# Optimization experiments

Measured on AMD Instinct MI355X. Metric: run time of the kernel, lower is better.

Reference implementation:

```python
import jax, jax.numpy as jnp
import numpy as np

N, IN_CH, OUT_CH, E = 16384, 512, 512, 8


def setup_inputs() -> dict:
    key = jax.random.key(0)
    k1, k2, k3, k4 = jax.random.split(key, 4)
    x = jax.random.normal(k1, (N, IN_CH), dtype=jnp.float32)
    coefficients = jax.random.uniform(k2, (N, E), dtype=jnp.float32)
    # kaiming-uniform-ish init: bound = 1/sqrt(fan_in)
    bound = 1.0 / np.sqrt(IN_CH)
    weight = jax.random.uniform(k3, (E, OUT_CH, IN_CH), minval=-bound, maxval=bound, dtype=jnp.float32)
    bias = jax.random.uniform(k4, (E, OUT_CH), minval=-bound, maxval=bound, dtype=jnp.float32)
    return {"x": x, "coefficients": coefficients, "weight": weight, "bias": bias}


def reference(x, coefficients, weight, bias):
    # Original: mixed_weight = einsum('bc,cmn->bmn', coef, W); out = baddbmm(mixed_bias, mixed_weight, x)
    # Equivalent (by bilinearity) without materializing the (N,out,in) tensor:
    # per-expert matvec combined with coefficients in one einsum.
    out = jnp.einsum('ne,eoi,ni->no', coefficients, weight, x)
    out = out + coefficients @ bias  # (N,E) @ (E,out) -> (N,out)
    return out
```

## Files before the change

### kernel.cpp

```cpp
#include <hip/hip_runtime.h>

#define N_TOK 16384
#define CIN   512
#define COUT  512
#define NE    8
#define BM    256
#define BN    128
#define BK    64
#define KTILES   64

typedef __attribute__((ext_vector_type(8))) short bf16x8;
typedef __attribute__((ext_vector_type(4))) short s16x4;
typedef __attribute__((ext_vector_type(4))) float f32x4;

__device__ __forceinline__ short f2bf(float f) {
  unsigned u = __builtin_bit_cast(unsigned, f);
  u += 0x7FFFu + ((u >> 16) & 1u);
  return (short)(u >> 16);
}

__global__ void cvt_all(const float4* __restrict__ x, const float4* __restrict__ w,
                        s16x4* __restrict__ xb, s16x4* __restrict__ wb) {
  int i = blockIdx.x * blockDim.x + threadIdx.x;
  const int NX = N_TOK * CIN / 4;
  float4 v; s16x4* o;
  if (i < NX) { v = x[i]; o = xb + i; }
  else       { int j = i - NX; v = w[j]; o = wb + j; }
  s16x4 r;
  r[0] = f2bf(v.x); r[1] = f2bf(v.y); r[2] = f2bf(v.z); r[3] = f2bf(v.w);
  *o = r;
}

__device__ __forceinline__ void async16(short* lds, const short* g) {
  __builtin_amdgcn_global_load_lds(
      (const __attribute__((address_space(1))) void*)g,
      (__attribute__((address_space(3))) void*)lds, 16, 0, 0);
}

__global__ __launch_bounds__(512, 2)
void moe_gemm(const short* __restrict__ xb,
              const short* __restrict__ wb,
              const float* __restrict__ coef,
              const float* __restrict__ bias,
              float* __restrict__ out) {
  __shared__ short As[3][BM * BK];
  __shared__ short Bs[3][BN * BK];
  __shared__ float cf[BM * NE];

  const int tid  = threadIdx.x;
  const int lane = tid & 63;
  const int wid  = tid >> 6;
  const int wm   = wid >> 2;
  const int wn   = wid & 3;
  const int lhi  = lane >> 4;
  const int llo  = lane & 15;

  const int bid  = blockIdx.x;
  const int ct   = bid & 3;
  const int rt   = bid >> 2;
  const int row0 = rt * BM;
  const int col0 = ct * BN;

  ((float4*)cf)[tid] = ((const float4*)(coef + row0 * NE))[tid];

  const int r_st = tid >> 3;
  const int c_sw = ((tid & 7) * 8) ^ ((r_st & 7) << 3);
  const short* gA = xb + (row0 + r_st) * CIN + c_sw;
  const short* gB = wb + (col0 + r_st) * CIN + c_sw;

  auto stageA = [&](int buf, int t, int p) {
    const int i0 = (t & 7) * BK;
    async16(&As[buf][p * 4096 + tid * 8], gA + p * 64 * CIN + i0);
  };
  auto stageB = [&](int buf, int t, int p) {
    const int e  = t >> 3;
    const int i0 = (t & 7) * BK;
    async16(&Bs[buf][p * 4096 + tid * 8], gB + e * (CIN * COUT) + p * 64 * CIN + i0);
  };

  const int swz0 = (lhi * 8) ^ ((llo & 7) << 3);
  const int swz1 = (32 + lhi * 8) ^ ((llo & 7) << 3);
  const int arow = wm * 128 + llo;
  const int brow = wn * 32 + llo;

  f32x4 accO[8][2], accE[8][2];
#pragma unroll
  for (int m = 0; m < 8; ++m)
#pragma unroll
    for (int n = 0; n < 2; ++n) {
      accO[m][n] = (f32x4){0.f, 0.f, 0.f, 0.f};
      accE[m][n] = (f32x4){0.f, 0.f, 0.f, 0.f};
    }

#pragma unroll
  for (int p = 0; p < 4; ++p) stageA(0, 0, p);
#pragma unroll
  for (int p = 0; p < 2; ++p) stageB(0, 0, p);
#pragma unroll
  for (int p = 0; p < 4; ++p) stageA(1, 1, p);
#pragma unroll
  for (int p = 0; p < 2; ++p) stageB(1, 1, p);
  asm volatile("s_waitcnt vmcnt(6) lgkmcnt(0)");
  __builtin_amdgcn_s_barrier();

  bf16x8 bfr[2][2];

  for (int t = 0; t < KTILES; ++t) {
    const int cur = t % 3;
    const int nx  = (t + 2) % 3;
    const bool pf = (t + 2) < KTILES;
    const short* Ab = As[cur];
    const short* Bb = Bs[cur];

#pragma unroll
    for (int p = 0; p < 4; ++p) {
      bf16x8 af[2][2];
      af[0][0] = *(const bf16x8*)&Ab[(arow + (2 * p) * 16) * 64 + swz0];
      af[0][1] = *(const bf16x8*)&Ab[(arow + (2 * p) * 16) * 64 + swz1];
      af[1][0] = *(const bf16x8*)&Ab[(arow + (2 * p + 1) * 16) * 64 + swz0];
      af[1][1] = *(const bf16x8*)&Ab[(arow + (2 * p + 1) * 16) * 64 + swz1];
      if (p == 0) {
        bfr[0][0] = *(const bf16x8*)&Bb[(brow + 0) * 64 + swz0];
        bfr[0][1] = *(const bf16x8*)&Bb[(brow + 0) * 64 + swz1];
        bfr[1][0] = *(const bf16x8*)&Bb[(brow + 16) * 64 + swz0];
        bfr[1][1] = *(const bf16x8*)&Bb[(brow + 16) * 64 + swz1];
      }
      if (pf) {
        if (p == 0)      { stageA(nx, t + 2, 0); stageA(nx, t + 2, 1); }
        else if (p == 1) { stageA(nx, t + 2, 2); stageA(nx, t + 2, 3); }
        else if (p == 2) { stageB(nx, t + 2, 0); stageB(nx, t + 2, 1); }
      }
      __builtin_amdgcn_s_barrier();
      asm volatile("s_waitcnt lgkmcnt(0)");
      __builtin_amdgcn_s_setprio(1);
#pragma unroll
      for (int mm = 0; mm < 2; ++mm)
#pragma unroll
        for (int n = 0; n < 2; ++n)
#pragma unroll
          for (int ks = 0; ks < 2; ++ks)
            accE[2 * p + mm][n] = __builtin_amdgcn_mfma_f32_16x16x32_bf16(
                af[mm][ks], bfr[n][ks], accE[2 * p + mm][n], 0, 0, 0);
      __builtin_amdgcn_s_setprio(0);
      __builtin_amdgcn_s_barrier();
    }

    if ((t & 7) == 7) {
      const int e = t >> 3;
#pragma unroll
      for (int m = 0; m < 8; ++m)
#pragma unroll
        for (int r = 0; r < 4; ++r) {
          float c = cf[(wm * 128 + m * 16 + lhi * 4 + r) * NE + e];
#pragma unroll
          for (int n = 0; n < 2; ++n) {
            accO[m][n][r] += c * accE[m][n][r];
            accE[m][n][r] = 0.f;
          }
        }
    }

    if (t < KTILES - 2) {
      asm volatile("s_waitcnt vmcnt(6)");
      __builtin_amdgcn_s_barrier();
    } else if (t == KTILES - 2) {
      asm volatile("s_waitcnt vmcnt(0)");
      __builtin_amdgcn_s_barrier();
    }
  }

  float bcol[2][NE];
#pragma unroll
  for (int n = 0; n < 2; ++n) {
    const int cg = col0 + wn * 32 + n * 16 + llo;
#pragma unroll
    for (int e = 0; e < NE; ++e) bcol[n][e] = bias[e * COUT + cg];
  }
#pragma unroll
  for (int m = 0; m < 8; ++m)
#pragma unroll
    for (int r = 0; r < 4; ++r) {
      const int rl = wm * 128 + m * 16 + lhi * 4 + r;
      float cv[NE];
#pragma unroll
      for (int e = 0; e < NE; ++e) cv[e] = cf[rl * NE + e];
      float* orow = out + (size_t)(row0 + rl) * COUT;
#pragma unroll
      for (int n = 0; n < 2; ++n) {
        float bm = 0.f;
#pragma unroll
        for (int e = 0; e < NE; ++e) bm += cv[e] * bcol[n][e];
        orow[col0 + wn * 32 + n * 16 + llo] = accO[m][n][r] + bm;
      }
    }
}

extern "C" void kernel_launch(void* const* d_in, const int* in_sizes, int n_in,
                              void* d_out, int out_size, void* d_ws, size_t ws_size,
                              hipStream_t stream) {
  const float* x    = (const float*)d_in[0];
  const float* coef = (const float*)d_in[1];
  const float* w    = (const float*)d_in[2];
  const float* bias = (const float*)d_in[3];
  float* out = (float*)d_out;

  short* xb = (short*)d_ws;
  short* wb = xb + (size_t)N_TOK * CIN;

  const int NX = N_TOK * CIN / 4, NW = NE * COUT * CIN / 4;
  cvt_all<<<(NX + NW) / 256, 256, 0, stream>>>(
      (const float4*)x, (const float4*)w, (s16x4*)xb, (s16x4*)wb);

  moe_gemm<<<(N_TOK / BM) * (COUT / BN), 512, 0, stream>>>(xb, wb, coef, bias, out);
}
```

Measured before the change: 192.5 us.

## Fold expert coefficients via Horner-style ratio rescaling, single accumulator set

Replaces the separate per-expert accumulator plus coefficient-weighted sum with one accumulator set. After each expert, the running sum is rescaled by the ratio c_e/c_{e+1}, and the last expert's coefficient is applied at the end. Precomputed ratios live in shared memory. The change also swaps the wave layout to 4x2 with 64x64 wave tiles, drops from triple to double buffering with a full vmcnt wait every tile, and adds a block-index swizzle. Fewer accumulator registers and less epilogue FMA work come at the cost of weaker load/compute overlap. Numerical risk: coefficients are clamped to 1e-20, and small coefficients give large ratios, so results depend on coefficients being positive and not near zero.

```diff
diff --git a/kernel.cpp b/kernel.cpp
--- a/kernel.cpp
+++ b/kernel.cpp
@@ -7,7 +7,7 @@
 #define BM    256
 #define BN    128
 #define BK    64
-#define KTILES   64
+#define KTILES 64
 
 typedef __attribute__((ext_vector_type(8))) short bf16x8;
 typedef __attribute__((ext_vector_type(4))) short s16x4;
@@ -43,154 +43,164 @@
               const float* __restrict__ coef,
               const float* __restrict__ bias,
               float* __restrict__ out) {
-  __shared__ short As[3][BM * BK];
-  __shared__ short Bs[3][BN * BK];
-  __shared__ float cf[BM * NE];
+  __shared__ short As[2][BM * BK];
+  __shared__ short Bs[2][BN * BK];
+  __shared__ float cfc[BM * NE];
+  __shared__ float cfr[BM * NE];
 
   const int tid  = threadIdx.x;
   const int lane = tid & 63;
   const int wid  = tid >> 6;
-  const int wm   = wid >> 2;
-  const int wn   = wid & 3;
+  const int wm   = wid >> 1;
+  const int wn   = wid & 1;
   const int lhi  = lane >> 4;
   const int llo  = lane & 15;
 
-  const int bid  = blockIdx.x;
+  const int bid0 = blockIdx.x;
+  const int bid  = (bid0 & 7) * 32 + (bid0 >> 3);
   const int ct   = bid & 3;
   const int rt   = bid >> 2;
   const int row0 = rt * BM;
   const int col0 = ct * BN;
 
-  ((float4*)cf)[tid] = ((const float4*)(coef + row0 * NE))[tid];
+  ((float4*)cfc)[tid] = ((const float4*)(coef + row0 * NE))[tid];
 
   const int r_st = tid >> 3;
   const int c_sw = ((tid & 7) * 8) ^ ((r_st & 7) << 3);
-  const short* gA = xb + (row0 + r_st) * CIN + c_sw;
-  const short* gB = wb + (col0 + r_st) * CIN + c_sw;
-
-  auto stageA = [&](int buf, int t, int p) {
-    const int i0 = (t & 7) * BK;
-    async16(&As[buf][p * 4096 + tid * 8], gA + p * 64 * CIN + i0);
-  };
-  auto stageB = [&](int buf, int t, int p) {
+  const short* gA = xb + (size_t)(row0 + r_st) * CIN + c_sw;
+  const short* gB = wb + (size_t)(col0 + r_st) * CIN + c_sw;
+
+  auto stage = [&](int buf, int t) {
     const int e  = t >> 3;
     const int i0 = (t & 7) * BK;
-    async16(&Bs[buf][p * 4096 + tid * 8], gB + e * (CIN * COUT) + p * 64 * CIN + i0);
+#pragma unroll
+    for (int p = 0; p < 4; ++p)
+      async16(&As[buf][p * 4096 + tid * 8], gA + p * 64 * CIN + i0);
+#pragma unroll
+    for (int p = 0; p < 2; ++p)
+      async16(&Bs[buf][p * 4096 + tid * 8], gB + (size_t)e * (CIN * COUT) + p * 64 * CIN + i0);
   };
+
+  stage(0, 0);
+  asm volatile("s_waitcnt lgkmcnt(0)");
+  __builtin_amdgcn_s_barrier();
+  if (tid < BM) {
+    const float* cp = &cfc[tid * NE];
+    float c[NE];
+#pragma unroll
+    for (int e = 0; e < NE; ++e) c[e] = fmaxf(cp[e], 1e-20f);
+    float* rp = &cfr[tid * NE];
+#pragma unroll
+    for (int e = 0; e < NE - 1; ++e) rp[e] = c[e] / c[e + 1];
+    rp[NE - 1] = c[NE - 1];
+  }
+  asm volatile("s_waitcnt vmcnt(0) lgkmcnt(0)");
+  __builtin_amdgcn_s_barrier();
 
   const int swz0 = (lhi * 8) ^ ((llo & 7) << 3);
   const int swz1 = (32 + lhi * 8) ^ ((llo & 7) << 3);
-  const int arow = wm * 128 + llo;
-  const int brow = wn * 32 + llo;
-
-  f32x4 accO[8][2], accE[8][2];
-#pragma unroll
-  for (int m = 0; m < 8; ++m)
-#pragma unroll
-    for (int n = 0; n < 2; ++n) {
-      accO[m][n] = (f32x4){0.f, 0.f, 0.f, 0.f};
-      accE[m][n] = (f32x4){0.f, 0.f, 0.f, 0.f};
-    }
-
-#pragma unroll
-  for (int p = 0; p < 4; ++p) stageA(0, 0, p);
-#pragma unroll
-  for (int p = 0; p < 2; ++p) stageB(0, 0, p);
-#pragma unroll
-  for (int p = 0; p < 4; ++p) stageA(1, 1, p);
-#pragma unroll
-  for (int p = 0; p < 2; ++p) stageB(1, 1, p);
-  asm volatile("s_waitcnt vmcnt(6) lgkmcnt(0)");
-  __builtin_amdgcn_s_barrier();
-
-  bf16x8 bfr[2][2];
+  const int arow = wm * 64 + llo;
+  const int brow = wn * 64 + llo;
+
+  f32x4 acc[4][4];
+#pragma unroll
+  for (int m = 0; m < 4; ++m)
+#pragma unroll
+    for (int n = 0; n < 4; ++n)
+      acc[m][n] = (f32x4){0.f, 0.f, 0.f, 0.f};
 
   for (int t = 0; t < KTILES; ++t) {
-    const int cur = t % 3;
-    const int nx  = (t + 2) % 3;
-    const bool pf = (t + 2) < KTILES;
+    const int cur = t & 1;
     const short* Ab = As[cur];
     const short* Bb = Bs[cur];
 
-#pragma unroll
-    for (int p = 0; p < 4; ++p) {
-      bf16x8 af[2][2];
-      af[0][0] = *(const bf16x8*)&Ab[(arow + (2 * p) * 16) * 64 + swz0];
-      af[0][1] = *(const bf16x8*)&Ab[(arow + (2 * p) * 16) * 64 + swz1];
-      af[1][0] = *(const bf16x8*)&Ab[(arow + (2 * p + 1) * 16) * 64 + swz0];
-      af[1][1] = *(const bf16x8*)&Ab[(arow + (2 * p + 1) * 16) * 64 + swz1];
-      if (p == 0) {
-        bfr[0][0] = *(const bf16x8*)&Bb[(brow + 0) * 64 + swz0];
-        bfr[0][1] = *(const bf16x8*)&Bb[(brow + 0) * 64 + swz1];
-        bfr[1][0] = *(const bf16x8*)&Bb[(brow + 16) * 64 + swz0];
-        bfr[1][1] = *(const bf16x8*)&Bb[(brow + 16) * 64 + swz1];
-      }
-      if (pf) {
-        if (p == 0)      { stageA(nx, t + 2, 0); stageA(nx, t + 2, 1); }
-        else if (p == 1) { stageA(nx, t + 2, 2); stageA(nx, t + 2, 3); }
-        else if (p == 2) { stageB(nx, t + 2, 0); stageB(nx, t + 2, 1); }
-      }
-      __builtin_amdgcn_s_barrier();
-      asm volatile("s_waitcnt lgkmcnt(0)");
-      __builtin_amdgcn_s_setprio(1);
-#pragma unroll
-      for (int mm = 0; mm < 2; ++mm)
-#pragma unroll
-        for (int n = 0; n < 2; ++n)
-#pragma unroll
-          for (int ks = 0; ks < 2; ++ks)
-            accE[2 * p + mm][n] = __builtin_amdgcn_mfma_f32_16x16x32_bf16(
-                af[mm][ks], bfr[n][ks], accE[2 * p + mm][n], 0, 0, 0);
-      __builtin_amdgcn_s_setprio(0);
-      __builtin_amdgcn_s_barrier();
-    }
+    if (t + 1 < KTILES) stage(cur ^ 1, t + 1);
+    bf16x8 bf[4][2];
+#pragma unroll
+    for (int n = 0; n < 4; ++n) {
+      bf[n][0] = *(const bf16x8*)&Bb[(brow + n * 16) * 64 + swz0];
+      bf[n][1] = *(const bf16x8*)&Bb[(brow + n * 16) * 64 + swz1];
+    }
+    bf16x8 af[2][2];
+#pragma unroll
+    for (int mm = 0; mm < 2; ++mm) {
+      af[mm][0] = *(const bf16x8*)&Ab[(arow + mm * 16) * 64 + swz0];
+      af[mm][1] = *(const bf16x8*)&Ab[(arow + mm * 16) * 64 + swz1];
+    }
+    __builtin_amdgcn_s_barrier();
+    asm volatile("s_waitcnt lgkmcnt(0)");
+    __builtin_amdgcn_s_setprio(1);
+#pragma unroll
+    for (int mm = 0; mm < 2; ++mm)
+#pragma unroll
+      for (int n = 0; n < 4; ++n)
+#pragma unroll
+        for (int ks = 0; ks < 2; ++ks)
+          acc[mm][n] = __builtin_amdgcn_mfma_f32_16x16x32_bf16(
+              af[mm][ks], bf[n][ks], acc[mm][n], 0, 0, 0);
+    __builtin_amdgcn_s_setprio(0);
+    __builtin_amdgcn_s_barrier();
+
+#pragma unroll
+    for (int mm = 0; mm < 2; ++mm) {
+      af[mm][0] = *(const bf16x8*)&Ab[(arow + (2 + mm) * 16) * 64 + swz0];
+      af[mm][1] = *(const bf16x8*)&Ab[(arow + (2 + mm) * 16) * 64 + swz1];
+    }
+    __builtin_amdgcn_s_barrier();
+    asm volatile("s_waitcnt lgkmcnt(0)");
+    __builtin_amdgcn_s_setprio(1);
+#pragma unroll
+    for (int mm = 0; mm < 2; ++mm)
+#pragma unroll
+      for (int n = 0; n < 4; ++n)
+#pragma unroll
+        for (int ks = 0; ks < 2; ++ks)
+          acc[2 + mm][n] = __builtin_amdgcn_mfma_f32_16x16x32_bf16(
+              af[mm][ks], bf[n][ks], acc[2 + mm][n], 0, 0, 0);
+    __builtin_amdgcn_s_setprio(0);
+    __builtin_amdgcn_s_barrier();
 
     if ((t & 7) == 7) {
       const int e = t >> 3;
 #pragma unroll
-      for (int m = 0; m < 8; ++m)
+      for (int m = 0; m < 4; ++m)
 #pragma unroll
         for (int r = 0; r < 4; ++r) {
-          float c = cf[(wm * 128 + m * 16 + lhi * 4 + r) * NE + e];
-#pragma unroll
-          for (int n = 0; n < 2; ++n) {
-            accO[m][n][r] += c * accE[m][n][r];
-            accE[m][n][r] = 0.f;
-          }
+          float rr = cfr[(wm * 64 + m * 16 + lhi * 4 + r) * NE + e];
+#pragma unroll
+          for (int n = 0; n < 4; ++n)
+            acc[m][n][r] *= rr;
         }
     }
 
-    if (t < KTILES - 2) {
-      asm volatile("s_waitcnt vmcnt(6)");
-      __builtin_amdgcn_s_barrier();
-    } else if (t == KTILES - 2) {
+    if (t + 1 < KTILES) {
       asm volatile("s_waitcnt vmcnt(0)");
       __builtin_amdgcn_s_barrier();
     }
   }
 
-  float bcol[2][NE];
-#pragma unroll
-  for (int n = 0; n < 2; ++n) {
-    const int cg = col0 + wn * 32 + n * 16 + llo;
+  float bcol[4][NE];
+#pragma unroll
+  for (int n = 0; n < 4; ++n) {
+    const int cg = col0 + wn * 64 + n * 16 + llo;
 #pragma unroll
     for (int e = 0; e < NE; ++e) bcol[n][e] = bias[e * COUT + cg];
   }
 #pragma unroll
-  for (int m = 0; m < 8; ++m)
+  for (int m = 0; m < 4; ++m)
 #pragma unroll
     for (int r = 0; r < 4; ++r) {
-      const int rl = wm * 128 + m * 16 + lhi * 4 + r;
+      const int rl = wm * 64 + m * 16 + lhi * 4 + r;
       float cv[NE];
 #pragma unroll
-      for (int e = 0; e < NE; ++e) cv[e] = cf[rl * NE + e];
+      for (int e = 0; e < NE; ++e) cv[e] = cfc[rl * NE + e];
       float* orow = out + (size_t)(row0 + rl) * COUT;
 #pragma unroll
-      for (int n = 0; n < 2; ++n) {
+      for (int n = 0; n < 4; ++n) {
         float bm = 0.f;
 #pragma unroll
         for (int e = 0; e < NE; ++e) bm += cv[e] * bcol[n][e];
-        orow[col0 + wn * 32 + n * 16 + llo] = accO[m][n][r] + bm;
+        orow[col0 + wn * 64 + n * 16 + llo] = acc[m][n][r] + bm;
       }
     }
 }
```

Result: faster. 183.6 us (-4.6%).
